# Optimization experiments

Hardware: AMD Instinct MI355X
Metric: run time of the kernel (lower is better)

## Reference

```python
import jax, jax.numpy as jnp
import numpy as np

DT = 1.0 / 120.0  # dt from init kwargs

def setup_inputs() -> dict:
    key = jax.random.key(0)
    k1, k2, k3, k4 = jax.random.split(key, 4)
    B, T = 4096, 4096
    u = jax.random.normal(k1, (B, T, 2), dtype=jnp.float32)
    x0 = jnp.zeros((B, 2), dtype=jnp.float32)
    k_w = jax.random.normal(k2, (1,), dtype=jnp.float32)
    b_w = jax.random.normal(k3, (1,), dtype=jnp.float32)
    input_mat = jax.random.normal(k4, (2, 2), dtype=jnp.float32)
    input_mask = jnp.ones((2, 2), dtype=jnp.float32)
    return {"u": u, "x0": x0, "k_w": k_w, "b_w": b_w,
            "input_mat": input_mat, "input_mask": input_mask}

def reference(u, x0, k_w, b_w, input_mat, input_mask):
    # log_train=False -> func = abs
    k = jnp.abs(k_w)  # (1,), broadcasts over batch
    b = jnp.abs(b_w)
    W = (input_mat * input_mask) * DT  # fold dt into input matrix
    u_t = jnp.swapaxes(u, 0, 1)  # [T, B, 2] time-major for scan

    def step(X, ut):
        x = X[:, 0]
        v = X[:, 1]
        x_new = x + v * DT
        v_new = v + (-k * x - b * v) * DT
        X_new = jnp.stack([x_new, v_new], axis=-1) + ut @ W  # [B, 2]
        return X_new, X_new

    _, ys = jax.lax.scan(step, x0, u_t)  # ys: [T, B, 2]
    return jnp.swapaxes(ys, 0, 1)  # [B, T, 2]
```

## Files before the change

kernel.cpp:

```cpp
#include <hip/hip_runtime.h>
#include <stdint.h>

#define DT (1.0f / 120.0f)

struct M2 { float a00, a01, a10, a11; };

__device__ __forceinline__ M2 mmul(const M2& x, const M2& y) {
    M2 r;
    r.a00 = x.a00 * y.a00 + x.a01 * y.a10;
    r.a01 = x.a00 * y.a01 + x.a01 * y.a11;
    r.a10 = x.a10 * y.a00 + x.a11 * y.a10;
    r.a11 = x.a10 * y.a01 + x.a11 * y.a11;
    return r;
}

__device__ __forceinline__ float2 vmul(float2 v, const M2& m) {
    return make_float2(v.x * m.a00 + v.y * m.a10,
                       v.x * m.a01 + v.y * m.a11);
}

#define GLOAD_LDS16(gp, lp) __builtin_amdgcn_global_load_lds(                 \
    (const __attribute__((address_space(1))) void*)(gp),                      \
    (__attribute__((address_space(3))) void*)(lp), 16, 0, 0)

template <int C, int BLOCK>
__global__ __launch_bounds__(BLOCK) void spring_scan(
    const float* __restrict__ u, const float* __restrict__ x0,
    const float* __restrict__ k_w, const float* __restrict__ b_w,
    const float* __restrict__ im, const float* __restrict__ imask,
    float* __restrict__ out, int T)
{
    static_assert(C == 16, "squaring count + swizzle assume C==16");
    constexpr int NW    = BLOCK / 64;
    constexpr int SLOTS = BLOCK * C / 2;
    constexpr int RNDS  = SLOTS / BLOCK;

    __shared__ float4 buf[SLOTS];
    __shared__ float2 lds_tot[NW];

    const int brow = blockIdx.x;
    const int tid  = threadIdx.x;
    const int lane = tid & 63;
    const int wid  = tid >> 6;

    const float k  = fabsf(k_w[0]);
    const float bd = fabsf(b_w[0]);
    const float W00 = im[0] * imask[0] * DT, W01 = im[1] * imask[1] * DT;
    const float W10 = im[2] * imask[2] * DT, W11 = im[3] * imask[3] * DT;

    M2 A = { 1.0f, -k * DT, DT, 1.0f - bd * DT };

    M2 P[7];
    {
        M2 t = A;
        #pragma unroll
        for (int i = 0; i < 4; ++i) t = mmul(t, t);
        P[0] = t;
        #pragma unroll
        for (int s = 1; s < 7; ++s) P[s] = mmul(P[s - 1], P[s - 1]);
    }
    M2 Mlane = { 1.f, 0.f, 0.f, 1.f };
    #pragma unroll
    for (int s = 0; s < 6; ++s)
        if ((lane >> s) & 1) Mlane = mmul(Mlane, P[s]);

    const long rowbase = (long)brow * T * 2;
    const float4* urow4 = (const float4*)(u + rowbase);
    float4*       orow4 = (float4*)(out + rowbase);

    float2 X_init = make_float2(x0[brow * 2 + 0], x0[brow * 2 + 1]);

    constexpr int STEPS = C * BLOCK;
    for (int t0 = 0; t0 < T; t0 += STEPS) {
        const int tilebase = t0 / 2;

        #pragma unroll
        for (int r = 0; r < RNDS; ++r) {
            const int p = r * BLOCK + tid;
            const int g = p ^ ((tid >> 3) & 7);
            GLOAD_LDS16(urow4 + tilebase + g, &buf[r * BLOCK + (tid & ~63)]);
        }
        __syncthreads();

        float2 c[C];
        #pragma unroll
        for (int m = 0; m < C / 2; ++m) {
            float4 t = buf[tid * (C / 2) + (m ^ (tid & 7))];
            c[2 * m + 0] = make_float2(t.x * W00 + t.y * W10,
                                       t.x * W01 + t.y * W11);
            c[2 * m + 1] = make_float2(t.z * W00 + t.w * W10,
                                       t.z * W01 + t.w * W11);
        }

        float2 v = make_float2(0.f, 0.f);
        #pragma unroll
        for (int i = 0; i < C; ++i) {
            v = vmul(v, A);
            v.x += c[i].x; v.y += c[i].y;
        }

        #pragma unroll
        for (int s = 0; s < 6; ++s) {
            float px = __shfl_up(v.x, 1u << s, 64);
            float py = __shfl_up(v.y, 1u << s, 64);
            if (lane >= (1 << s)) {
                float2 pv = vmul(make_float2(px, py), P[s]);
                v.x = pv.x + v.x; v.y = pv.y + v.y;
            }
        }

        if (lane == 63) lds_tot[wid] = v;
        __syncthreads();

        float2 off = X_init;
        for (int w2 = 0; w2 < wid; ++w2) {
            off = vmul(off, P[6]);
            off.x += lds_tot[w2].x; off.y += lds_tot[w2].y;
        }

        float ex = __shfl_up(v.x, 1u, 64);
        float ey = __shfl_up(v.y, 1u, 64);
        float2 vex = (lane == 0) ? make_float2(0.f, 0.f) : make_float2(ex, ey);

        float2 X = vmul(off, Mlane);
        X.x += vex.x; X.y += vex.y;

        #pragma unroll
        for (int m = 0; m < C / 2; ++m) {
            float4 o;
            X = vmul(X, A);
            X.x += c[2 * m + 0].x; X.y += c[2 * m + 0].y;
            o.x = X.x; o.y = X.y;
            X = vmul(X, A);
            X.x += c[2 * m + 1].x; X.y += c[2 * m + 1].y;
            o.z = X.x; o.w = X.y;
            buf[tid * (C / 2) + (m ^ (tid & 7))] = o;
        }
        __syncthreads();

        #pragma unroll
        for (int r = 0; r < RNDS; ++r) {
            const int p = r * BLOCK + tid;
            const int g = p ^ ((tid >> 3) & 7);
            orow4[tilebase + g] = buf[p];
        }

        if (t0 + STEPS < T) {
            float2 fin = X_init;
            #pragma unroll
            for (int w2 = 0; w2 < NW; ++w2) {
                fin = vmul(fin, P[6]);
                fin.x += lds_tot[w2].x; fin.y += lds_tot[w2].y;
            }
            X_init = fin;
            __syncthreads();
        }
    }
}

extern "C" void kernel_launch(void* const* d_in, const int* in_sizes, int n_in,
                              void* d_out, int out_size, void* d_ws, size_t ws_size,
                              hipStream_t stream) {
    const float* u     = (const float*)d_in[0];
    const float* x0    = (const float*)d_in[1];
    const float* k_w   = (const float*)d_in[2];
    const float* b_w   = (const float*)d_in[3];
    const float* im    = (const float*)d_in[4];
    const float* imask = (const float*)d_in[5];
    float* out = (float*)d_out;

    const int B = in_sizes[1] / 2;
    const int T = in_sizes[0] / (2 * B);

    spring_scan<16, 256><<<B, 256, 0, stream>>>(u, x0, k_w, b_w, im, imask, out, T);
}
```

Before: 46.80 us.

## Prefetch next tile into LDS per-wave and drop block barrier before global loads

Measured after the change: 47.61 us. About the same (+1.7%).

```diff
diff --git a/kernel.cpp b/kernel.cpp
--- a/kernel.cpp
+++ b/kernel.cpp
@@ -31,17 +31,30 @@
     float* __restrict__ out, int T)
 {
     static_assert(C == 16, "squaring count + swizzle assume C==16");
-    constexpr int NW    = BLOCK / 64;
-    constexpr int SLOTS = BLOCK * C / 2;
-    constexpr int RNDS  = SLOTS / BLOCK;
+    constexpr int NW     = BLOCK / 64;
+    constexpr int SLOTS  = BLOCK * C / 2;
+    constexpr int WSLOTS = 64 * C / 2;
 
     __shared__ float4 buf[SLOTS];
-    __shared__ float2 lds_tot[NW];
 
     const int brow = blockIdx.x;
     const int tid  = threadIdx.x;
     const int lane = tid & 63;
     const int wid  = tid >> 6;
+    const int wbase = wid * WSLOTS;
+
+    const long rowbase = (long)brow * T * 2;
+    const float4* urow4 = (const float4*)(u + rowbase);
+    float4*       orow4 = (float4*)(out + rowbase);
+
+    constexpr int STEPS = C * BLOCK;
+
+    {
+        const int lsw = lane ^ (lane >> 3);
+        #pragma unroll
+        for (int j = 0; j < C / 2; ++j)
+            GLOAD_LDS16(urow4 + wbase + j * 64 + lsw, &buf[wbase + j * 64]);
+    }
 
     const float k  = fabsf(k_w[0]);
     const float bd = fabsf(b_w[0]);
@@ -64,28 +77,18 @@
     for (int s = 0; s < 6; ++s)
         if ((lane >> s) & 1) Mlane = mmul(Mlane, P[s]);
 
-    const long rowbase = (long)brow * T * 2;
-    const float4* urow4 = (const float4*)(u + rowbase);
-    float4*       orow4 = (float4*)(out + rowbase);
-
     float2 X_init = make_float2(x0[brow * 2 + 0], x0[brow * 2 + 1]);
 
-    constexpr int STEPS = C * BLOCK;
     for (int t0 = 0; t0 < T; t0 += STEPS) {
         const int tilebase = t0 / 2;
 
-        #pragma unroll
-        for (int r = 0; r < RNDS; ++r) {
-            const int p = r * BLOCK + tid;
-            const int g = p ^ ((tid >> 3) & 7);
-            GLOAD_LDS16(urow4 + tilebase + g, &buf[r * BLOCK + (tid & ~63)]);
-        }
-        __syncthreads();
+        asm volatile("s_waitcnt vmcnt(0)" ::: "memory");
+        __builtin_amdgcn_sched_barrier(0);
 
         float2 c[C];
         #pragma unroll
         for (int m = 0; m < C / 2; ++m) {
-            float4 t = buf[tid * (C / 2) + (m ^ (tid & 7))];
+            float4 t = buf[wbase + lane * (C / 2) + (m ^ (lane & 7))];
             c[2 * m + 0] = make_float2(t.x * W00 + t.y * W10,
                                        t.x * W01 + t.y * W11);
             c[2 * m + 1] = make_float2(t.z * W00 + t.w * W10,
@@ -109,13 +112,26 @@
             }
         }
 
-        if (lane == 63) lds_tot[wid] = v;
+        if (lane == 63) *(float2*)&buf[wbase] = v;
         __syncthreads();
 
         float2 off = X_init;
         for (int w2 = 0; w2 < wid; ++w2) {
             off = vmul(off, P[6]);
-            off.x += lds_tot[w2].x; off.y += lds_tot[w2].y;
+            float2 tw = *(const float2*)&buf[w2 * WSLOTS];
+            off.x += tw.x; off.y += tw.y;
+        }
+
+        const bool carry = (t0 + STEPS < T);
+        float2 fin;
+        if (carry) {
+            fin = X_init;
+            #pragma unroll
+            for (int w2 = 0; w2 < NW; ++w2) {
+                fin = vmul(fin, P[6]);
+                float2 tw = *(const float2*)&buf[w2 * WSLOTS];
+                fin.x += tw.x; fin.y += tw.y;
+            }
         }
 
         float ex = __shfl_up(v.x, 1u, 64);
@@ -124,6 +140,8 @@
 
         float2 X = vmul(off, Mlane);
         X.x += vex.x; X.y += vex.y;
+
+        __syncthreads();
 
         #pragma unroll
         for (int m = 0; m < C / 2; ++m) {
@@ -134,26 +152,24 @@
             X = vmul(X, A);
             X.x += c[2 * m + 1].x; X.y += c[2 * m + 1].y;
             o.z = X.x; o.w = X.y;
-            buf[tid * (C / 2) + (m ^ (tid & 7))] = o;
-        }
-        __syncthreads();
-
-        #pragma unroll
-        for (int r = 0; r < RNDS; ++r) {
-            const int p = r * BLOCK + tid;
-            const int g = p ^ ((tid >> 3) & 7);
-            orow4[tilebase + g] = buf[p];
+            buf[wbase + lane * (C / 2) + (m ^ (lane & 7))] = o;
         }
 
-        if (t0 + STEPS < T) {
-            float2 fin = X_init;
+        {
+            const int lsw = lane ^ (lane >> 3);
             #pragma unroll
-            for (int w2 = 0; w2 < NW; ++w2) {
-                fin = vmul(fin, P[6]);
-                fin.x += lds_tot[w2].x; fin.y += lds_tot[w2].y;
-            }
+            for (int j = 0; j < C / 2; ++j)
+                orow4[tilebase + wbase + j * 64 + lsw] = buf[wbase + j * 64 + lane];
+        }
+
+        if (carry) {
             X_init = fin;
             __syncthreads();
+            const int lsw = lane ^ (lane >> 3);
+            const int nb  = tilebase + SLOTS;
+            #pragma unroll
+            for (int j = 0; j < C / 2; ++j)
+                GLOAD_LDS16(urow4 + nb + wbase + j * 64 + lsw, &buf[wbase + j * 64]);
         }
     }
 }
```
